# Performance work log

Hardware: AMD Instinct MI355X
Metric: run time of the kernel (lower is better)

## Reference

```python
import jax, jax.numpy as jnp
import numpy as np

N_NODES = 50000
N_EDGES = 800000
DIM_IN = 128
DIM_OUT = 64


def setup_inputs() -> dict:
    key = jax.random.key(0)
    k1, k2, k3, k4 = jax.random.split(key, 4)
    x = jax.random.normal(k1, (N_NODES, DIM_IN), dtype=jnp.float32)
    edge_index = jax.random.randint(k2, (2, N_EDGES), 0, N_NODES, dtype=jnp.int64)
    W = jax.random.normal(k3, (DIM_IN, DIM_OUT), dtype=jnp.float32) / np.sqrt(DIM_IN)
    b = jax.random.normal(k4, (DIM_OUT,), dtype=jnp.float32) * 0.01
    return {"x": x, "edge_index": edge_index, "W": W, "b": b}


def reference(x, edge_index, W, b):
    # Faithful PyG GCNConv: add self-loops, symmetric deg normalization,
    # linear transform then normalized scatter-add aggregation, then bias.
    N = x.shape[0]
    h = x @ W  # [N, dim_out] — transform before propagate (PyG order)

    loops = jnp.arange(N, dtype=edge_index.dtype)
    src = jnp.concatenate([edge_index[0], loops])  # [E+N]
    dst = jnp.concatenate([edge_index[1], loops])  # [E+N]

    ones = jnp.ones(src.shape[0], dtype=h.dtype)
    deg = jax.ops.segment_sum(ones, dst, num_segments=N)  # in-degree incl. self-loop
    dinv = jnp.where(deg > 0, jax.lax.rsqrt(deg), 0.0)
    norm = dinv[src] * dinv[dst]  # [E+N]

    msgs = h[src] * norm[:, None]  # gather + scale
    out = jax.ops.segment_sum(msgs, dst, num_segments=N) + b  # scatter-add
    return jax.nn.log_softmax(out, axis=1)
```

## Files before the change

### kernel.cpp

```cpp
#include <hip/hip_runtime.h>
#include <hip/hip_fp16.h>
#include <cstdint>
#include <cstddef>

#define N_NODES 50000
#define N_EDGES 800000
#define DIM_IN  128
#define DIM_OUT 64

#define BSHIFT  6
#define BNODES  64
#define NB      1024
#define NBK     ((N_NODES + BNODES - 1) / BNODES)
#define EB      4096
#define SORTB   ((N_EDGES + EB - 1) / EB)
#define NE4     (N_EDGES / 4)
#define CAPB    1280
#define GROWS   128

typedef _Float16 f16x8 __attribute__((ext_vector_type(8)));
typedef _Float16 f16x4 __attribute__((ext_vector_type(4)));
typedef float    f32x4 __attribute__((ext_vector_type(4)));

__global__ __launch_bounds__(256) void k_zero(int* __restrict__ gcnt) {
    const int i = blockIdx.x * 256 + threadIdx.x;
    if (i < NB) gcnt[i] = 0;
}

__global__ __launch_bounds__(256) void kF(const int* __restrict__ ei,
                                          int* __restrict__ gcnt,
                                          unsigned* __restrict__ pairs) {
    __shared__ int hcnt[NB];
    __shared__ int cur[NB];
    const int t = threadIdx.x, blk = blockIdx.x;
    for (int i = t; i < NB; i += 256) hcnt[i] = 0;
    __syncthreads();

    const int4* src4 = (const int4*)ei;
    const int4* dst4 = (const int4*)(ei + N_EDGES);
    const int g0 = blk * (EB / 4);

#pragma unroll
    for (int it = 0; it < EB / 1024; ++it) {
        const int g = g0 + it * 256 + t;
        if (g < NE4) {
            const int4 d = dst4[g];
            atomicAdd(&hcnt[d.x >> BSHIFT], 1);
            atomicAdd(&hcnt[d.y >> BSHIFT], 1);
            atomicAdd(&hcnt[d.z >> BSHIFT], 1);
            atomicAdd(&hcnt[d.w >> BSHIFT], 1);
        }
    }
    __syncthreads();

    for (int i = t; i < NB; i += 256) {
        const int c = hcnt[i];
        const int base = c ? atomicAdd(&gcnt[i], c) : 0;
        cur[i] = i * CAPB + base;
    }
    __syncthreads();

#pragma unroll
    for (int it = 0; it < EB / 1024; ++it) {
        const int g = g0 + it * 256 + t;
        if (g < NE4) {
            const int4 sv = src4[g];
            const int4 dv = dst4[g];
            int b, p;
            b = dv.x >> BSHIFT; p = atomicAdd(&cur[b], 1);
            if (p < b * CAPB + CAPB) pairs[p] = ((unsigned)sv.x << 16) | (unsigned)dv.x;
            b = dv.y >> BSHIFT; p = atomicAdd(&cur[b], 1);
            if (p < b * CAPB + CAPB) pairs[p] = ((unsigned)sv.y << 16) | (unsigned)dv.y;
            b = dv.z >> BSHIFT; p = atomicAdd(&cur[b], 1);
            if (p < b * CAPB + CAPB) pairs[p] = ((unsigned)sv.z << 16) | (unsigned)dv.z;
            b = dv.w >> BSHIFT; p = atomicAdd(&cur[b], 1);
            if (p < b * CAPB + CAPB) pairs[p] = ((unsigned)sv.w << 16) | (unsigned)dv.w;
        }
    }
}

__global__ __launch_bounds__(256) void kSort(const unsigned* __restrict__ pairs,
                                             const int* __restrict__ gcnt,
                                             unsigned short* __restrict__ csr,
                                             int2* __restrict__ nodeoff2,
                                             float* __restrict__ dinv) {
    __shared__ int cnt[BNODES];
    __shared__ int cur[BNODES];
    const int b = blockIdx.x, t = threadIdx.x;
    const int eb = b * CAPB;
    const int count = min(gcnt[b], CAPB);
    const int ee = eb + count;

    if (t < BNODES) cnt[t] = 0;
    __syncthreads();

    {
        int i = eb + t;
        for (; i + 768 < ee; i += 1024) {
            const unsigned p0 = pairs[i];
            const unsigned p1 = pairs[i + 256];
            const unsigned p2 = pairs[i + 512];
            const unsigned p3 = pairs[i + 768];
            atomicAdd(&cnt[p0 & (BNODES - 1)], 1);
            atomicAdd(&cnt[p1 & (BNODES - 1)], 1);
            atomicAdd(&cnt[p2 & (BNODES - 1)], 1);
            atomicAdd(&cnt[p3 & (BNODES - 1)], 1);
        }
        for (; i < ee; i += 256) atomicAdd(&cnt[pairs[i] & (BNODES - 1)], 1);
    }
    __syncthreads();

    if (t < 64) {
        const int lane = t;
        const int v = cnt[lane];
        int xs = v;
#pragma unroll
        for (int off = 1; off < 64; off <<= 1) {
            int y = __shfl_up(xs, off);
            if (lane >= off) xs += y;
        }
        const int excl = xs - v;
        cur[lane] = eb + excl;
        const int n = (b << BSHIFT) + lane;
        if (n < N_NODES) {
            nodeoff2[n] = make_int2(eb + excl, v);
            dinv[n] = rsqrtf((float)(v + 1));
        }
    }
    __syncthreads();

    {
        int i = eb + t;
        for (; i + 768 < ee; i += 1024) {
            const unsigned p0 = pairs[i];
            const unsigned p1 = pairs[i + 256];
            const unsigned p2 = pairs[i + 512];
            const unsigned p3 = pairs[i + 768];
            int q;
            q = atomicAdd(&cur[p0 & (BNODES - 1)], 1); csr[q] = (unsigned short)(p0 >> 16);
            q = atomicAdd(&cur[p1 & (BNODES - 1)], 1); csr[q] = (unsigned short)(p1 >> 16);
            q = atomicAdd(&cur[p2 & (BNODES - 1)], 1); csr[q] = (unsigned short)(p2 >> 16);
            q = atomicAdd(&cur[p3 & (BNODES - 1)], 1); csr[q] = (unsigned short)(p3 >> 16);
        }
        for (; i < ee; i += 256) {
            const unsigned p = pairs[i];
            const int q = atomicAdd(&cur[p & (BNODES - 1)], 1);
            csr[q] = (unsigned short)(p >> 16);
        }
    }
}

__global__ __launch_bounds__(256) void k_gemm(const float* __restrict__ x,
                                              const float* __restrict__ W,
                                              const float* __restrict__ dinv,
                                              __half* __restrict__ h) {
    const int t = threadIdx.x;
    const int w = t >> 6;
    const int l = t & 63;
    const int q = l >> 4;
    const int m16 = l & 15;

    f16x8 bf[4][4];
#pragma unroll
    for (int kc = 0; kc < 4; ++kc)
#pragma unroll
        for (int ct = 0; ct < 4; ++ct) {
            const float* wp = W + (size_t)(kc * 32 + q * 8) * DIM_OUT + ct * 16 + m16;
            f16x8 v;
#pragma unroll
            for (int j = 0; j < 8; ++j) v[j] = (_Float16)wp[(size_t)j * DIM_OUT];
            bf[kc][ct] = v;
        }

    const int base = blockIdx.x * GROWS + w * 32;
#pragma unroll
    for (int rt = 0; rt < 2; ++rt) {
        const int m0 = base + rt * 16;
        int mrow = m0 + m16;
        if (mrow >= N_NODES) mrow = N_NODES - 1;

        f16x8 af[4];
#pragma unroll
        for (int kc = 0; kc < 4; ++kc) {
            const float4* xp = (const float4*)(x + (size_t)mrow * DIM_IN + kc * 32 + q * 8);
            const float4 p0 = xp[0], p1 = xp[1];
            f16x8 a;
            a[0] = (_Float16)p0.x; a[1] = (_Float16)p0.y;
            a[2] = (_Float16)p0.z; a[3] = (_Float16)p0.w;
            a[4] = (_Float16)p1.x; a[5] = (_Float16)p1.y;
            a[6] = (_Float16)p1.z; a[7] = (_Float16)p1.w;
            af[kc] = a;
        }

        f32x4 acc[4];
#pragma unroll
        for (int ct = 0; ct < 4; ++ct) acc[ct] = (f32x4){0.f, 0.f, 0.f, 0.f};
#pragma unroll
        for (int kc = 0; kc < 4; ++kc)
#pragma unroll
            for (int ct = 0; ct < 4; ++ct)
                acc[ct] = __builtin_amdgcn_mfma_f32_16x16x32_f16(af[kc], bf[kc][ct], acc[ct], 0, 0, 0);

#pragma unroll
        for (int reg = 0; reg < 4; ++reg) {
            const int r = m0 + q * 4 + reg;
            if (r < N_NODES) {
                const float d = dinv[r];
#pragma unroll
                for (int ct = 0; ct < 4; ++ct)
                    h[(size_t)r * DIM_OUT + ct * 16 + m16] = __float2half(acc[ct][reg] * d);
            }
        }
    }
}

__global__ __launch_bounds__(256) void kE_agg(const int2* __restrict__ nodeoff2,
                                              const unsigned short* __restrict__ csr,
                                              const __half* __restrict__ h,
                                              const float* __restrict__ bvec,
                                              float* __restrict__ out) {
    const int t = threadIdx.x;
    const int qw = t >> 4, sl = t & 15;
    const int n = blockIdx.x * 16 + qw;
    const f16x4* __restrict__ h4 = (const f16x4*)h;

    const int2 off = nodeoff2[n];
    const int s0 = off.x, s1 = off.x + off.y;

    const f16x4 hv = h4[n * 16 + sl];
    float a0f = (float)hv[0], a1f = (float)hv[1], a2f = (float)hv[2], a3f = (float)hv[3];

    int i = s0;
    for (; i + 4 <= s1; i += 4) {
        const int c0 = csr[i + 0];
        const int c1 = csr[i + 1];
        const int c2 = csr[i + 2];
        const int c3 = csr[i + 3];
        const f16x4 v0 = h4[c0 * 16 + sl];
        const f16x4 v1 = h4[c1 * 16 + sl];
        const f16x4 v2 = h4[c2 * 16 + sl];
        const f16x4 v3 = h4[c3 * 16 + sl];
        a0f += (float)v0[0] + (float)v1[0] + (float)v2[0] + (float)v3[0];
        a1f += (float)v0[1] + (float)v1[1] + (float)v2[1] + (float)v3[1];
        a2f += (float)v0[2] + (float)v1[2] + (float)v2[2] + (float)v3[2];
        a3f += (float)v0[3] + (float)v1[3] + (float)v2[3] + (float)v3[3];
    }
    for (; i < s1; ++i) {
        const f16x4 v0 = h4[csr[i] * 16 + sl];
        a0f += (float)v0[0]; a1f += (float)v0[1]; a2f += (float)v0[2]; a3f += (float)v0[3];
    }

    const float4 bias = *(const float4*)&bvec[4 * sl];
    const float di = rsqrtf((float)(off.y + 1));
    float v0 = a0f * di + bias.x;
    float v1 = a1f * di + bias.y;
    float v2 = a2f * di + bias.z;
    float v3 = a3f * di + bias.w;

    float m = fmaxf(fmaxf(v0, v1), fmaxf(v2, v3));
#pragma unroll
    for (int off2 = 8; off2 > 0; off2 >>= 1) m = fmaxf(m, __shfl_xor(m, off2));
    float s = __expf(v0 - m) + __expf(v1 - m) + __expf(v2 - m) + __expf(v3 - m);
#pragma unroll
    for (int off2 = 8; off2 > 0; off2 >>= 1) s += __shfl_xor(s, off2);
    const float ls = __logf(s);

    float4 o;
    o.x = v0 - m - ls; o.y = v1 - m - ls; o.z = v2 - m - ls; o.w = v3 - m - ls;
    *(float4*)&out[(size_t)n * DIM_OUT + 4 * sl] = o;
}

extern "C" void kernel_launch(void* const* d_in, const int* in_sizes, int n_in,
                              void* d_out, int out_size, void* d_ws, size_t ws_size,
                              hipStream_t stream) {
    const float* x  = (const float*)d_in[0];
    const int*   ei = (const int*)d_in[1];
    const float* W  = (const float*)d_in[2];
    const float* b  = (const float*)d_in[3];
    float* out = (float*)d_out;

    char* ws = (char*)d_ws;
    __half*         h        = (__half*)ws;         ws += (size_t)N_NODES * DIM_OUT * sizeof(__half);
    float*          dinv     = (float*)ws;          ws += (size_t)N_NODES * sizeof(float);
    unsigned*       pairs    = (unsigned*)ws;       ws += (size_t)NB * CAPB * sizeof(unsigned);
    unsigned short* csr      = (unsigned short*)ws; ws += (size_t)NB * CAPB * sizeof(unsigned short);
    int2*           nodeoff2 = (int2*)ws;           ws += (size_t)N_NODES * sizeof(int2);
    int*            gcnt     = (int*)ws;            ws += (size_t)NB * sizeof(int);

    k_zero<<<(NB + 255) / 256, 256, 0, stream>>>(gcnt);
    kF    <<<SORTB, 256, 0, stream>>>(ei, gcnt, pairs);
    kSort <<<NBK, 256, 0, stream>>>(pairs, gcnt, csr, nodeoff2, dinv);
    k_gemm<<<(N_NODES + GROWS - 1) / GROWS, 256, 0, stream>>>(x, W, dinv, h);
    kE_agg<<<N_NODES / 16, 256, 0, stream>>>(nodeoff2, csr, h, b, out);
}
```

Measured before the change: 123.5 us.

## Fuse all GCN stages into one persistent cooperative kernel with grid syncs

Replaces the five separate launches (zero, bucket scatter, per-bucket sort, GEMM, aggregate) with one cooperative persistent kernel that loops over work units and uses grid.sync between phases. The bucket scatter and the GEMM now run in the same phase, and the dinv scaling of h moves into the sort phase as a read-modify-write pass. This removes launch gaps and lets the edge binning overlap the GEMM. In exchange it adds grid-wide barriers, an extra read and write of h, and a fixed grid of up to 3x256 blocks that may limit occupancy during the aggregation phase.

```diff
diff --git a/kernel.cpp b/kernel.cpp
--- a/kernel.cpp
+++ b/kernel.cpp
@@ -1,7 +1,10 @@
 #include <hip/hip_runtime.h>
 #include <hip/hip_fp16.h>
+#include <hip/hip_cooperative_groups.h>
 #include <cstdint>
 #include <cstddef>
+
+namespace cg = cooperative_groups;
 
 #define N_NODES 50000
 #define N_EDGES 800000
@@ -17,257 +20,278 @@
 #define NE4     (N_EDGES / 4)
 #define CAPB    1280
 #define GROWS   128
+#define GEMMB   ((N_NODES + GROWS - 1) / GROWS)
+#define P1UNITS (SORTB + GEMMB)
+#define NGROUP  (N_NODES / 16)
 
 typedef _Float16 f16x8 __attribute__((ext_vector_type(8)));
 typedef _Float16 f16x4 __attribute__((ext_vector_type(4)));
 typedef float    f32x4 __attribute__((ext_vector_type(4)));
 
-__global__ __launch_bounds__(256) void k_zero(int* __restrict__ gcnt) {
-    const int i = blockIdx.x * 256 + threadIdx.x;
-    if (i < NB) gcnt[i] = 0;
-}
-
-__global__ __launch_bounds__(256) void kF(const int* __restrict__ ei,
-                                          int* __restrict__ gcnt,
-                                          unsigned* __restrict__ pairs) {
-    __shared__ int hcnt[NB];
-    __shared__ int cur[NB];
-    const int t = threadIdx.x, blk = blockIdx.x;
-    for (int i = t; i < NB; i += 256) hcnt[i] = 0;
-    __syncthreads();
-
-    const int4* src4 = (const int4*)ei;
-    const int4* dst4 = (const int4*)(ei + N_EDGES);
-    const int g0 = blk * (EB / 4);
-
-#pragma unroll
-    for (int it = 0; it < EB / 1024; ++it) {
-        const int g = g0 + it * 256 + t;
-        if (g < NE4) {
-            const int4 d = dst4[g];
-            atomicAdd(&hcnt[d.x >> BSHIFT], 1);
-            atomicAdd(&hcnt[d.y >> BSHIFT], 1);
-            atomicAdd(&hcnt[d.z >> BSHIFT], 1);
-            atomicAdd(&hcnt[d.w >> BSHIFT], 1);
+__global__ __launch_bounds__(256, 3) void kFused(
+        const int* __restrict__ ei,
+        int* __restrict__ gcnt,
+        unsigned* __restrict__ pairs,
+        const float* __restrict__ x,
+        const float* __restrict__ W,
+        unsigned short* __restrict__ csr,
+        int2* __restrict__ nodeoff2,
+        __half* __restrict__ h,
+        const float* __restrict__ bvec,
+        float* __restrict__ out) {
+    cg::grid_group grid = cg::this_grid();
+    const int t = threadIdx.x;
+    const int blk = blockIdx.x;
+    const int gsz = (int)gridDim.x;
+
+    __shared__ int sA[NB];
+    __shared__ int sB[NB];
+
+    if (blk < 4) gcnt[blk * 256 + t] = 0;
+    grid.sync();
+
+    for (int u = blk; u < P1UNITS; u += gsz) {
+        if (u < SORTB) {
+            __syncthreads();
+            for (int i = t; i < NB; i += 256) sA[i] = 0;
+            __syncthreads();
+            const int4* src4 = (const int4*)ei;
+            const int4* dst4 = (const int4*)(ei + N_EDGES);
+            const int g0 = u * (EB / 4);
+#pragma unroll
+            for (int it = 0; it < EB / 1024; ++it) {
+                const int g = g0 + it * 256 + t;
+                if (g < NE4) {
+                    const int4 d = dst4[g];
+                    atomicAdd(&sA[d.x >> BSHIFT], 1);
+                    atomicAdd(&sA[d.y >> BSHIFT], 1);
+                    atomicAdd(&sA[d.z >> BSHIFT], 1);
+                    atomicAdd(&sA[d.w >> BSHIFT], 1);
+                }
+            }
+            __syncthreads();
+            for (int i = t; i < NB; i += 256) {
+                const int c = sA[i];
+                const int base = c ? atomicAdd(&gcnt[i], c) : 0;
+                sB[i] = i * CAPB + base;
+            }
+            __syncthreads();
+#pragma unroll
+            for (int it = 0; it < EB / 1024; ++it) {
+                const int g = g0 + it * 256 + t;
+                if (g < NE4) {
+                    const int4 sv = src4[g];
+                    const int4 dv = dst4[g];
+                    int b, p;
+                    b = dv.x >> BSHIFT; p = atomicAdd(&sB[b], 1);
+                    if (p < b * CAPB + CAPB) pairs[p] = ((unsigned)sv.x << 16) | (unsigned)dv.x;
+                    b = dv.y >> BSHIFT; p = atomicAdd(&sB[b], 1);
+                    if (p < b * CAPB + CAPB) pairs[p] = ((unsigned)sv.y << 16) | (unsigned)dv.y;
+                    b = dv.z >> BSHIFT; p = atomicAdd(&sB[b], 1);
+                    if (p < b * CAPB + CAPB) pairs[p] = ((unsigned)sv.z << 16) | (unsigned)dv.z;
+                    b = dv.w >> BSHIFT; p = atomicAdd(&sB[b], 1);
+                    if (p < b * CAPB + CAPB) pairs[p] = ((unsigned)sv.w << 16) | (unsigned)dv.w;
+                }
+            }
+            __syncthreads();
+        } else {
+            const int w = t >> 6;
+            const int l = t & 63;
+            const int q = l >> 4;
+            const int m16 = l & 15;
+
+            f16x8 bf[4][4];
+#pragma unroll
+            for (int kc = 0; kc < 4; ++kc)
+#pragma unroll
+                for (int ct = 0; ct < 4; ++ct) {
+                    const float* wp = W + (size_t)(kc * 32 + q * 8) * DIM_OUT + ct * 16 + m16;
+                    f16x8 v;
+#pragma unroll
+                    for (int j = 0; j < 8; ++j) v[j] = (_Float16)wp[(size_t)j * DIM_OUT];
+                    bf[kc][ct] = v;
+                }
+
+            const int base = (u - SORTB) * GROWS + w * 32;
+#pragma unroll
+            for (int rt = 0; rt < 2; ++rt) {
+                const int m0 = base + rt * 16;
+                int mrow = m0 + m16;
+                if (mrow >= N_NODES) mrow = N_NODES - 1;
+
+                f16x8 af[4];
+#pragma unroll
+                for (int kc = 0; kc < 4; ++kc) {
+                    const float4* xp = (const float4*)(x + (size_t)mrow * DIM_IN + kc * 32 + q * 8);
+                    const float4 p0 = xp[0], p1 = xp[1];
+                    f16x8 a;
+                    a[0] = (_Float16)p0.x; a[1] = (_Float16)p0.y;
+                    a[2] = (_Float16)p0.z; a[3] = (_Float16)p0.w;
+                    a[4] = (_Float16)p1.x; a[5] = (_Float16)p1.y;
+                    a[6] = (_Float16)p1.z; a[7] = (_Float16)p1.w;
+                    af[kc] = a;
+                }
+
+                f32x4 acc[4];
+#pragma unroll
+                for (int ct = 0; ct < 4; ++ct) acc[ct] = (f32x4){0.f, 0.f, 0.f, 0.f};
+#pragma unroll
+                for (int kc = 0; kc < 4; ++kc)
+#pragma unroll
+                    for (int ct = 0; ct < 4; ++ct)
+                        acc[ct] = __builtin_amdgcn_mfma_f32_16x16x32_f16(af[kc], bf[kc][ct], acc[ct], 0, 0, 0);
+
+#pragma unroll
+                for (int reg = 0; reg < 4; ++reg) {
+                    const int r = m0 + q * 4 + reg;
+                    if (r < N_NODES) {
+#pragma unroll
+                        for (int ct = 0; ct < 4; ++ct)
+                            h[(size_t)r * DIM_OUT + ct * 16 + m16] = __float2half(acc[ct][reg]);
+                    }
+                }
+            }
         }
     }
-    __syncthreads();
-
-    for (int i = t; i < NB; i += 256) {
-        const int c = hcnt[i];
-        const int base = c ? atomicAdd(&gcnt[i], c) : 0;
-        cur[i] = i * CAPB + base;
-    }
-    __syncthreads();
-
-#pragma unroll
-    for (int it = 0; it < EB / 1024; ++it) {
-        const int g = g0 + it * 256 + t;
-        if (g < NE4) {
-            const int4 sv = src4[g];
-            const int4 dv = dst4[g];
-            int b, p;
-            b = dv.x >> BSHIFT; p = atomicAdd(&cur[b], 1);
-            if (p < b * CAPB + CAPB) pairs[p] = ((unsigned)sv.x << 16) | (unsigned)dv.x;
-            b = dv.y >> BSHIFT; p = atomicAdd(&cur[b], 1);
-            if (p < b * CAPB + CAPB) pairs[p] = ((unsigned)sv.y << 16) | (unsigned)dv.y;
-            b = dv.z >> BSHIFT; p = atomicAdd(&cur[b], 1);
-            if (p < b * CAPB + CAPB) pairs[p] = ((unsigned)sv.z << 16) | (unsigned)dv.z;
-            b = dv.w >> BSHIFT; p = atomicAdd(&cur[b], 1);
-            if (p < b * CAPB + CAPB) pairs[p] = ((unsigned)sv.w << 16) | (unsigned)dv.w;
+    grid.sync();
+
+    {
+        int* cnt = sA;
+        int* cur = sA + BNODES;
+        float* sdinv = (float*)(sA + 2 * BNODES);
+        f16x4* h4w = (f16x4*)h;
+
+        for (int bb = blk; bb < NBK; bb += gsz) {
+            __syncthreads();
+            if (t < BNODES) cnt[t] = 0;
+            __syncthreads();
+
+            const int eb = bb * CAPB;
+            const int count = min(gcnt[bb], CAPB);
+            const int ee = eb + count;
+
+            {
+                int i = eb + t;
+                for (; i + 768 < ee; i += 1024) {
+                    const unsigned p0 = pairs[i];
+                    const unsigned p1 = pairs[i + 256];
+                    const unsigned p2 = pairs[i + 512];
+                    const unsigned p3 = pairs[i + 768];
+                    atomicAdd(&cnt[p0 & (BNODES - 1)], 1);
+                    atomicAdd(&cnt[p1 & (BNODES - 1)], 1);
+                    atomicAdd(&cnt[p2 & (BNODES - 1)], 1);
+                    atomicAdd(&cnt[p3 & (BNODES - 1)], 1);
+                }
+                for (; i < ee; i += 256) atomicAdd(&cnt[pairs[i] & (BNODES - 1)], 1);
+            }
+            __syncthreads();
+
+            if (t < 64) {
+                const int lane = t;
+                const int v = cnt[lane];
+                int xs = v;
+#pragma unroll
+                for (int off = 1; off < 64; off <<= 1) {
+                    int y = __shfl_up(xs, off);
+                    if (lane >= off) xs += y;
+                }
+                const int excl = xs - v;
+                cur[lane] = eb + excl;
+                sdinv[lane] = rsqrtf((float)(v + 1));
+                const int n = (bb << BSHIFT) + lane;
+                if (n < N_NODES) nodeoff2[n] = make_int2(eb + excl, v);
+            }
+            __syncthreads();
+
+            for (int idx = t; idx < BNODES * 16; idx += 256) {
+                const int r = idx >> 4;
+                const int n = (bb << BSHIFT) + r;
+                if (n < N_NODES) {
+                    const float d = sdinv[r];
+                    f16x4 v = h4w[n * 16 + (idx & 15)];
+                    v[0] = (_Float16)((float)v[0] * d);
+                    v[1] = (_Float16)((float)v[1] * d);
+                    v[2] = (_Float16)((float)v[2] * d);
+                    v[3] = (_Float16)((float)v[3] * d);
+                    h4w[n * 16 + (idx & 15)] = v;
+                }
+            }
+
+            {
+                int i = eb + t;
+                for (; i + 768 < ee; i += 1024) {
+                    const unsigned p0 = pairs[i];
+                    const unsigned p1 = pairs[i + 256];
+                    const unsigned p2 = pairs[i + 512];
+                    const unsigned p3 = pairs[i + 768];
+                    int q;
+                    q = atomicAdd(&cur[p0 & (BNODES - 1)], 1); csr[q] = (unsigned short)(p0 >> 16);
+                    q = atomicAdd(&cur[p1 & (BNODES - 1)], 1); csr[q] = (unsigned short)(p1 >> 16);
+                    q = atomicAdd(&cur[p2 & (BNODES - 1)], 1); csr[q] = (unsigned short)(p2 >> 16);
+                    q = atomicAdd(&cur[p3 & (BNODES - 1)], 1); csr[q] = (unsigned short)(p3 >> 16);
+                }
+                for (; i < ee; i += 256) {
+                    const unsigned p = pairs[i];
+                    const int q = atomicAdd(&cur[p & (BNODES - 1)], 1);
+                    csr[q] = (unsigned short)(p >> 16);
+                }
+            }
         }
     }
-}
-
-__global__ __launch_bounds__(256) void kSort(const unsigned* __restrict__ pairs,
-                                             const int* __restrict__ gcnt,
-                                             unsigned short* __restrict__ csr,
-                                             int2* __restrict__ nodeoff2,
-                                             float* __restrict__ dinv) {
-    __shared__ int cnt[BNODES];
-    __shared__ int cur[BNODES];
-    const int b = blockIdx.x, t = threadIdx.x;
-    const int eb = b * CAPB;
-    const int count = min(gcnt[b], CAPB);
-    const int ee = eb + count;
-
-    if (t < BNODES) cnt[t] = 0;
-    __syncthreads();
+    grid.sync();
 
     {
-        int i = eb + t;
-        for (; i + 768 < ee; i += 1024) {
-            const unsigned p0 = pairs[i];
-            const unsigned p1 = pairs[i + 256];
-            const unsigned p2 = pairs[i + 512];
-            const unsigned p3 = pairs[i + 768];
-            atomicAdd(&cnt[p0 & (BNODES - 1)], 1);
-            atomicAdd(&cnt[p1 & (BNODES - 1)], 1);
-            atomicAdd(&cnt[p2 & (BNODES - 1)], 1);
-            atomicAdd(&cnt[p3 & (BNODES - 1)], 1);
-        }
-        for (; i < ee; i += 256) atomicAdd(&cnt[pairs[i] & (BNODES - 1)], 1);
-    }
-    __syncthreads();
-
-    if (t < 64) {
-        const int lane = t;
-        const int v = cnt[lane];
-        int xs = v;
-#pragma unroll
-        for (int off = 1; off < 64; off <<= 1) {
-            int y = __shfl_up(xs, off);
-            if (lane >= off) xs += y;
-        }
-        const int excl = xs - v;
-        cur[lane] = eb + excl;
-        const int n = (b << BSHIFT) + lane;
-        if (n < N_NODES) {
-            nodeoff2[n] = make_int2(eb + excl, v);
-            dinv[n] = rsqrtf((float)(v + 1));
+        const int qw = t >> 4, sl = t & 15;
+        const f16x4* __restrict__ h4 = (const f16x4*)h;
+        const float4 bias = *(const float4*)&bvec[4 * sl];
+
+        for (int g = blk; g < NGROUP; g += gsz) {
+            const int n = g * 16 + qw;
+            const int2 off = nodeoff2[n];
+            const int s0 = off.x, s1 = off.x + off.y;
+
+            const f16x4 hv = h4[n * 16 + sl];
+            float a0f = (float)hv[0], a1f = (float)hv[1], a2f = (float)hv[2], a3f = (float)hv[3];
+
+            int i = s0;
+            for (; i + 4 <= s1; i += 4) {
+                const int c0 = csr[i + 0];
+                const int c1 = csr[i + 1];
+                const int c2 = csr[i + 2];
+                const int c3 = csr[i + 3];
+                const f16x4 v0 = h4[c0 * 16 + sl];
+                const f16x4 v1 = h4[c1 * 16 + sl];
+                const f16x4 v2 = h4[c2 * 16 + sl];
+                const f16x4 v3 = h4[c3 * 16 + sl];
+                a0f += (float)v0[0] + (float)v1[0] + (float)v2[0] + (float)v3[0];
+                a1f += (float)v0[1] + (float)v1[1] + (float)v2[1] + (float)v3[1];
+                a2f += (float)v0[2] + (float)v1[2] + (float)v2[2] + (float)v3[2];
+                a3f += (float)v0[3] + (float)v1[3] + (float)v2[3] + (float)v3[3];
+            }
+            for (; i < s1; ++i) {
+                const f16x4 v0 = h4[csr[i] * 16 + sl];
+                a0f += (float)v0[0]; a1f += (float)v0[1]; a2f += (float)v0[2]; a3f += (float)v0[3];
+            }
+
+            const float di = rsqrtf((float)(off.y + 1));
+            float v0 = a0f * di + bias.x;
+            float v1 = a1f * di + bias.y;
+            float v2 = a2f * di + bias.z;
+            float v3 = a3f * di + bias.w;
+
+            float m = fmaxf(fmaxf(v0, v1), fmaxf(v2, v3));
+#pragma unroll
+            for (int o = 8; o > 0; o >>= 1) m = fmaxf(m, __shfl_xor(m, o));
+            float s = __expf(v0 - m) + __expf(v1 - m) + __expf(v2 - m) + __expf(v3 - m);
+#pragma unroll
+            for (int o = 8; o > 0; o >>= 1) s += __shfl_xor(s, o);
+            const float ls = __logf(s);
+
+            float4 o4;
+            o4.x = v0 - m - ls; o4.y = v1 - m - ls; o4.z = v2 - m - ls; o4.w = v3 - m - ls;
+            *(float4*)&out[(size_t)n * DIM_OUT + 4 * sl] = o4;
         }
     }
-    __syncthreads();
-
-    {
-        int i = eb + t;
-        for (; i + 768 < ee; i += 1024) {
-            const unsigned p0 = pairs[i];
-            const unsigned p1 = pairs[i + 256];
-            const unsigned p2 = pairs[i + 512];
-            const unsigned p3 = pairs[i + 768];
-            int q;
-            q = atomicAdd(&cur[p0 & (BNODES - 1)], 1); csr[q] = (unsigned short)(p0 >> 16);
-            q = atomicAdd(&cur[p1 & (BNODES - 1)], 1); csr[q] = (unsigned short)(p1 >> 16);
-            q = atomicAdd(&cur[p2 & (BNODES - 1)], 1); csr[q] = (unsigned short)(p2 >> 16);
-            q = atomicAdd(&cur[p3 & (BNODES - 1)], 1); csr[q] = (unsigned short)(p3 >> 16);
-        }
-        for (; i < ee; i += 256) {
-            const unsigned p = pairs[i];
-            const int q = atomicAdd(&cur[p & (BNODES - 1)], 1);
-            csr[q] = (unsigned short)(p >> 16);
-        }
-    }
-}
-
-__global__ __launch_bounds__(256) void k_gemm(const float* __restrict__ x,
-                                              const float* __restrict__ W,
-                                              const float* __restrict__ dinv,
-                                              __half* __restrict__ h) {
-    const int t = threadIdx.x;
-    const int w = t >> 6;
-    const int l = t & 63;
-    const int q = l >> 4;
-    const int m16 = l & 15;
-
-    f16x8 bf[4][4];
-#pragma unroll
-    for (int kc = 0; kc < 4; ++kc)
-#pragma unroll
-        for (int ct = 0; ct < 4; ++ct) {
-            const float* wp = W + (size_t)(kc * 32 + q * 8) * DIM_OUT + ct * 16 + m16;
-            f16x8 v;
-#pragma unroll
-            for (int j = 0; j < 8; ++j) v[j] = (_Float16)wp[(size_t)j * DIM_OUT];
-            bf[kc][ct] = v;
-        }
-
-    const int base = blockIdx.x * GROWS + w * 32;
-#pragma unroll
-    for (int rt = 0; rt < 2; ++rt) {
-        const int m0 = base + rt * 16;
-        int mrow = m0 + m16;
-        if (mrow >= N_NODES) mrow = N_NODES - 1;
-
-        f16x8 af[4];
-#pragma unroll
-        for (int kc = 0; kc < 4; ++kc) {
-            const float4* xp = (const float4*)(x + (size_t)mrow * DIM_IN + kc * 32 + q * 8);
-            const float4 p0 = xp[0], p1 = xp[1];
-            f16x8 a;
-            a[0] = (_Float16)p0.x; a[1] = (_Float16)p0.y;
-            a[2] = (_Float16)p0.z; a[3] = (_Float16)p0.w;
-            a[4] = (_Float16)p1.x; a[5] = (_Float16)p1.y;
-            a[6] = (_Float16)p1.z; a[7] = (_Float16)p1.w;
-            af[kc] = a;
-        }
-
-        f32x4 acc[4];
-#pragma unroll
-        for (int ct = 0; ct < 4; ++ct) acc[ct] = (f32x4){0.f, 0.f, 0.f, 0.f};
-#pragma unroll
-        for (int kc = 0; kc < 4; ++kc)
-#pragma unroll
-            for (int ct = 0; ct < 4; ++ct)
-                acc[ct] = __builtin_amdgcn_mfma_f32_16x16x32_f16(af[kc], bf[kc][ct], acc[ct], 0, 0, 0);
-
-#pragma unroll
-        for (int reg = 0; reg < 4; ++reg) {
-            const int r = m0 + q * 4 + reg;
-            if (r < N_NODES) {
-                const float d = dinv[r];
-#pragma unroll
-                for (int ct = 0; ct < 4; ++ct)
-                    h[(size_t)r * DIM_OUT + ct * 16 + m16] = __float2half(acc[ct][reg] * d);
-            }
-        }
-    }
-}
-
-__global__ __launch_bounds__(256) void kE_agg(const int2* __restrict__ nodeoff2,
-                                              const unsigned short* __restrict__ csr,
-                                              const __half* __restrict__ h,
-                                              const float* __restrict__ bvec,
-                                              float* __restrict__ out) {
-    const int t = threadIdx.x;
-    const int qw = t >> 4, sl = t & 15;
-    const int n = blockIdx.x * 16 + qw;
-    const f16x4* __restrict__ h4 = (const f16x4*)h;
-
-    const int2 off = nodeoff2[n];
-    const int s0 = off.x, s1 = off.x + off.y;
-
-    const f16x4 hv = h4[n * 16 + sl];
-    float a0f = (float)hv[0], a1f = (float)hv[1], a2f = (float)hv[2], a3f = (float)hv[3];
-
-    int i = s0;
-    for (; i + 4 <= s1; i += 4) {
-        const int c0 = csr[i + 0];
-        const int c1 = csr[i + 1];
-        const int c2 = csr[i + 2];
-        const int c3 = csr[i + 3];
-        const f16x4 v0 = h4[c0 * 16 + sl];
-        const f16x4 v1 = h4[c1 * 16 + sl];
-        const f16x4 v2 = h4[c2 * 16 + sl];
-        const f16x4 v3 = h4[c3 * 16 + sl];
-        a0f += (float)v0[0] + (float)v1[0] + (float)v2[0] + (float)v3[0];
-        a1f += (float)v0[1] + (float)v1[1] + (float)v2[1] + (float)v3[1];
-        a2f += (float)v0[2] + (float)v1[2] + (float)v2[2] + (float)v3[2];
-        a3f += (float)v0[3] + (float)v1[3] + (float)v2[3] + (float)v3[3];
-    }
-    for (; i < s1; ++i) {
-        const f16x4 v0 = h4[csr[i] * 16 + sl];
-        a0f += (float)v0[0]; a1f += (float)v0[1]; a2f += (float)v0[2]; a3f += (float)v0[3];
-    }
-
-    const float4 bias = *(const float4*)&bvec[4 * sl];
-    const float di = rsqrtf((float)(off.y + 1));
-    float v0 = a0f * di + bias.x;
-    float v1 = a1f * di + bias.y;
-    float v2 = a2f * di + bias.z;
-    float v3 = a3f * di + bias.w;
-
-    float m = fmaxf(fmaxf(v0, v1), fmaxf(v2, v3));
-#pragma unroll
-    for (int off2 = 8; off2 > 0; off2 >>= 1) m = fmaxf(m, __shfl_xor(m, off2));
-    float s = __expf(v0 - m) + __expf(v1 - m) + __expf(v2 - m) + __expf(v3 - m);
-#pragma unroll
-    for (int off2 = 8; off2 > 0; off2 >>= 1) s += __shfl_xor(s, off2);
-    const float ls = __logf(s);
-
-    float4 o;
-    o.x = v0 - m - ls; o.y = v1 - m - ls; o.z = v2 - m - ls; o.w = v3 - m - ls;
-    *(float4*)&out[(size_t)n * DIM_OUT + 4 * sl] = o;
 }
 
 extern "C" void kernel_launch(void* const* d_in, const int* in_sizes, int n_in,
@@ -281,15 +305,19 @@
 
     char* ws = (char*)d_ws;
     __half*         h        = (__half*)ws;         ws += (size_t)N_NODES * DIM_OUT * sizeof(__half);
-    float*          dinv     = (float*)ws;          ws += (size_t)N_NODES * sizeof(float);
     unsigned*       pairs    = (unsigned*)ws;       ws += (size_t)NB * CAPB * sizeof(unsigned);
     unsigned short* csr      = (unsigned short*)ws; ws += (size_t)NB * CAPB * sizeof(unsigned short);
     int2*           nodeoff2 = (int2*)ws;           ws += (size_t)N_NODES * sizeof(int2);
     int*            gcnt     = (int*)ws;            ws += (size_t)NB * sizeof(int);
 
-    k_zero<<<(NB + 255) / 256, 256, 0, stream>>>(gcnt);
-    kF    <<<SORTB, 256, 0, stream>>>(ei, gcnt, pairs);
-    kSort <<<NBK, 256, 0, stream>>>(pairs, gcnt, csr, nodeoff2, dinv);
-    k_gemm<<<(N_NODES + GROWS - 1) / GROWS, 256, 0, stream>>>(x, W, dinv, h);
-    kE_agg<<<N_NODES / 16, 256, 0, stream>>>(nodeoff2, csr, h, b, out);
+    int maxb = 0;
+    (void)hipOccupancyMaxActiveBlocksPerMultiprocessor(&maxb, kFused, 256, 0);
+    if (maxb < 1) maxb = 1;
+    if (maxb > 3) maxb = 3;
+    const int grid = maxb * 256;
+
+    void* args[] = {(void*)&ei, (void*)&gcnt, (void*)&pairs, (void*)&x, (void*)&W,
+                    (void*)&csr, (void*)&nodeoff2, (void*)&h, (void*)&b, (void*)&out};
+    (void)hipLaunchCooperativeKernel((void*)kFused, dim3(grid), dim3(256),
+                                     args, 0, stream);
 }
```

Result: slower. 305.4 us (+147.2%).

## Fuse edge binning with GEMM and apply dinv scaling in sort kernel

Applied to the files above, without the earlier changes.

The edge-binning pass and the x@W GEMM now run as one launch, with block ranges split by blockIdx, so the independent GEMM can overlap the atomic-heavy binning. The GEMM no longer depends on dinv. The per-node dinv scaling of h moves into kSort, which computes degrees and rescales its 64 rows of h in place. The aggregation kernel now uses 8 lanes per node with f16x8 loads instead of 16 lanes with f16x4. This drops one launch and the dinv buffer, but adds a read-modify-write of h in kSort and a second fp16 rounding of h.

```diff
diff --git a/kernel.cpp b/kernel.cpp
--- a/kernel.cpp
+++ b/kernel.cpp
@@ -17,6 +17,8 @@
 #define NE4     (N_EDGES / 4)
 #define CAPB    1280
 #define GROWS   128
+#define GEMMB   ((N_NODES + GROWS - 1) / GROWS)
+#define NEGRP   ((N_NODES + 31) / 32)
 
 typedef _Float16 f16x8 __attribute__((ext_vector_type(8)));
 typedef _Float16 f16x4 __attribute__((ext_vector_type(4)));
@@ -27,54 +29,114 @@
     if (i < NB) gcnt[i] = 0;
 }
 
-__global__ __launch_bounds__(256) void kF(const int* __restrict__ ei,
-                                          int* __restrict__ gcnt,
-                                          unsigned* __restrict__ pairs) {
-    __shared__ int hcnt[NB];
-    __shared__ int cur[NB];
-    const int t = threadIdx.x, blk = blockIdx.x;
-    for (int i = t; i < NB; i += 256) hcnt[i] = 0;
-    __syncthreads();
-
-    const int4* src4 = (const int4*)ei;
-    const int4* dst4 = (const int4*)(ei + N_EDGES);
-    const int g0 = blk * (EB / 4);
-
-#pragma unroll
-    for (int it = 0; it < EB / 1024; ++it) {
-        const int g = g0 + it * 256 + t;
-        if (g < NE4) {
-            const int4 d = dst4[g];
-            atomicAdd(&hcnt[d.x >> BSHIFT], 1);
-            atomicAdd(&hcnt[d.y >> BSHIFT], 1);
-            atomicAdd(&hcnt[d.z >> BSHIFT], 1);
-            atomicAdd(&hcnt[d.w >> BSHIFT], 1);
-        }
-    }
-    __syncthreads();
-
-    for (int i = t; i < NB; i += 256) {
-        const int c = hcnt[i];
-        const int base = c ? atomicAdd(&gcnt[i], c) : 0;
-        cur[i] = i * CAPB + base;
-    }
-    __syncthreads();
-
-#pragma unroll
-    for (int it = 0; it < EB / 1024; ++it) {
-        const int g = g0 + it * 256 + t;
-        if (g < NE4) {
-            const int4 sv = src4[g];
-            const int4 dv = dst4[g];
-            int b, p;
-            b = dv.x >> BSHIFT; p = atomicAdd(&cur[b], 1);
-            if (p < b * CAPB + CAPB) pairs[p] = ((unsigned)sv.x << 16) | (unsigned)dv.x;
-            b = dv.y >> BSHIFT; p = atomicAdd(&cur[b], 1);
-            if (p < b * CAPB + CAPB) pairs[p] = ((unsigned)sv.y << 16) | (unsigned)dv.y;
-            b = dv.z >> BSHIFT; p = atomicAdd(&cur[b], 1);
-            if (p < b * CAPB + CAPB) pairs[p] = ((unsigned)sv.z << 16) | (unsigned)dv.z;
-            b = dv.w >> BSHIFT; p = atomicAdd(&cur[b], 1);
-            if (p < b * CAPB + CAPB) pairs[p] = ((unsigned)sv.w << 16) | (unsigned)dv.w;
+__global__ __launch_bounds__(256) void kFG(const int* __restrict__ ei,
+                                           int* __restrict__ gcnt,
+                                           unsigned* __restrict__ pairs,
+                                           const float* __restrict__ x,
+                                           const float* __restrict__ W,
+                                           __half* __restrict__ h) {
+    const int t = threadIdx.x;
+    if (blockIdx.x < SORTB) {
+        __shared__ int hcnt[NB];
+        __shared__ int cur[NB];
+        const int blk = blockIdx.x;
+        for (int i = t; i < NB; i += 256) hcnt[i] = 0;
+        __syncthreads();
+        const int4* src4 = (const int4*)ei;
+        const int4* dst4 = (const int4*)(ei + N_EDGES);
+        const int g0 = blk * (EB / 4);
+#pragma unroll
+        for (int it = 0; it < EB / 1024; ++it) {
+            const int g = g0 + it * 256 + t;
+            if (g < NE4) {
+                const int4 d = dst4[g];
+                atomicAdd(&hcnt[d.x >> BSHIFT], 1);
+                atomicAdd(&hcnt[d.y >> BSHIFT], 1);
+                atomicAdd(&hcnt[d.z >> BSHIFT], 1);
+                atomicAdd(&hcnt[d.w >> BSHIFT], 1);
+            }
+        }
+        __syncthreads();
+        for (int i = t; i < NB; i += 256) {
+            const int c = hcnt[i];
+            const int base = c ? atomicAdd(&gcnt[i], c) : 0;
+            cur[i] = i * CAPB + base;
+        }
+        __syncthreads();
+#pragma unroll
+        for (int it = 0; it < EB / 1024; ++it) {
+            const int g = g0 + it * 256 + t;
+            if (g < NE4) {
+                const int4 sv = src4[g];
+                const int4 dv = dst4[g];
+                int b, p;
+                b = dv.x >> BSHIFT; p = atomicAdd(&cur[b], 1);
+                if (p < b * CAPB + CAPB) pairs[p] = ((unsigned)sv.x << 16) | (unsigned)dv.x;
+                b = dv.y >> BSHIFT; p = atomicAdd(&cur[b], 1);
+                if (p < b * CAPB + CAPB) pairs[p] = ((unsigned)sv.y << 16) | (unsigned)dv.y;
+                b = dv.z >> BSHIFT; p = atomicAdd(&cur[b], 1);
+                if (p < b * CAPB + CAPB) pairs[p] = ((unsigned)sv.z << 16) | (unsigned)dv.z;
+                b = dv.w >> BSHIFT; p = atomicAdd(&cur[b], 1);
+                if (p < b * CAPB + CAPB) pairs[p] = ((unsigned)sv.w << 16) | (unsigned)dv.w;
+            }
+        }
+    } else {
+        const int u = blockIdx.x - SORTB;
+        const int w = t >> 6;
+        const int l = t & 63;
+        const int q = l >> 4;
+        const int m16 = l & 15;
+
+        f16x8 bf[4][4];
+#pragma unroll
+        for (int kc = 0; kc < 4; ++kc)
+#pragma unroll
+            for (int ct = 0; ct < 4; ++ct) {
+                const float* wp = W + (size_t)(kc * 32 + q * 8) * DIM_OUT + ct * 16 + m16;
+                f16x8 v;
+#pragma unroll
+                for (int j = 0; j < 8; ++j) v[j] = (_Float16)wp[(size_t)j * DIM_OUT];
+                bf[kc][ct] = v;
+            }
+
+        const int base = u * GROWS + w * 32;
+#pragma unroll
+        for (int rt = 0; rt < 2; ++rt) {
+            const int m0 = base + rt * 16;
+            int mrow = m0 + m16;
+            if (mrow >= N_NODES) mrow = N_NODES - 1;
+
+            f16x8 af[4];
+#pragma unroll
+            for (int kc = 0; kc < 4; ++kc) {
+                const float4* xp = (const float4*)(x + (size_t)mrow * DIM_IN + kc * 32 + q * 8);
+                const float4 p0 = xp[0], p1 = xp[1];
+                f16x8 a;
+                a[0] = (_Float16)p0.x; a[1] = (_Float16)p0.y;
+                a[2] = (_Float16)p0.z; a[3] = (_Float16)p0.w;
+                a[4] = (_Float16)p1.x; a[5] = (_Float16)p1.y;
+                a[6] = (_Float16)p1.z; a[7] = (_Float16)p1.w;
+                af[kc] = a;
+            }
+
+            f32x4 acc[4];
+#pragma unroll
+            for (int ct = 0; ct < 4; ++ct) acc[ct] = (f32x4){0.f, 0.f, 0.f, 0.f};
+#pragma unroll
+            for (int kc = 0; kc < 4; ++kc)
+#pragma unroll
+                for (int ct = 0; ct < 4; ++ct)
+                    acc[ct] = __builtin_amdgcn_mfma_f32_16x16x32_f16(af[kc], bf[kc][ct], acc[ct], 0, 0, 0);
+
+#pragma unroll
+            for (int reg = 0; reg < 4; ++reg) {
+                const int r = m0 + q * 4 + reg;
+                if (r < N_NODES) {
+#pragma unroll
+                    for (int ct = 0; ct < 4; ++ct)
+                        h[(size_t)r * DIM_OUT + ct * 16 + m16] = __float2half(acc[ct][reg]);
+                }
+            }
         }
     }
 }
@@ -83,9 +145,10 @@
                                              const int* __restrict__ gcnt,
                                              unsigned short* __restrict__ csr,
                                              int2* __restrict__ nodeoff2,
-                                             float* __restrict__ dinv) {
+                                             __half* __restrict__ h) {
     __shared__ int cnt[BNODES];
     __shared__ int cur[BNODES];
+    __shared__ float sdinv[BNODES];
     const int b = blockIdx.x, t = threadIdx.x;
     const int eb = b * CAPB;
     const int count = min(gcnt[b], CAPB);
@@ -121,13 +184,26 @@
         }
         const int excl = xs - v;
         cur[lane] = eb + excl;
+        sdinv[lane] = rsqrtf((float)(v + 1));
         const int n = (b << BSHIFT) + lane;
-        if (n < N_NODES) {
-            nodeoff2[n] = make_int2(eb + excl, v);
-            dinv[n] = rsqrtf((float)(v + 1));
-        }
+        if (n < N_NODES) nodeoff2[n] = make_int2(eb + excl, v);
     }
     __syncthreads();
+
+    {
+        f16x8* h8w = (f16x8*)h;
+        for (int idx = t; idx < BNODES * 8; idx += 256) {
+            const int r = idx >> 3;
+            const int n = (b << BSHIFT) + r;
+            if (n < N_NODES) {
+                const float d = sdinv[r];
+                f16x8 v = h8w[n * 8 + (idx & 7)];
+#pragma unroll
+                for (int j = 0; j < 8; ++j) v[j] = (_Float16)((float)v[j] * d);
+                h8w[n * 8 + (idx & 7)] = v;
+            }
+        }
+    }
 
     {
         int i = eb + t;
@@ -150,85 +226,24 @@
     }
 }
 
-__global__ __launch_bounds__(256) void k_gemm(const float* __restrict__ x,
-                                              const float* __restrict__ W,
-                                              const float* __restrict__ dinv,
-                                              __half* __restrict__ h) {
-    const int t = threadIdx.x;
-    const int w = t >> 6;
-    const int l = t & 63;
-    const int q = l >> 4;
-    const int m16 = l & 15;
-
-    f16x8 bf[4][4];
-#pragma unroll
-    for (int kc = 0; kc < 4; ++kc)
-#pragma unroll
-        for (int ct = 0; ct < 4; ++ct) {
-            const float* wp = W + (size_t)(kc * 32 + q * 8) * DIM_OUT + ct * 16 + m16;
-            f16x8 v;
-#pragma unroll
-            for (int j = 0; j < 8; ++j) v[j] = (_Float16)wp[(size_t)j * DIM_OUT];
-            bf[kc][ct] = v;
-        }
-
-    const int base = blockIdx.x * GROWS + w * 32;
-#pragma unroll
-    for (int rt = 0; rt < 2; ++rt) {
-        const int m0 = base + rt * 16;
-        int mrow = m0 + m16;
-        if (mrow >= N_NODES) mrow = N_NODES - 1;
-
-        f16x8 af[4];
-#pragma unroll
-        for (int kc = 0; kc < 4; ++kc) {
-            const float4* xp = (const float4*)(x + (size_t)mrow * DIM_IN + kc * 32 + q * 8);
-            const float4 p0 = xp[0], p1 = xp[1];
-            f16x8 a;
-            a[0] = (_Float16)p0.x; a[1] = (_Float16)p0.y;
-            a[2] = (_Float16)p0.z; a[3] = (_Float16)p0.w;
-            a[4] = (_Float16)p1.x; a[5] = (_Float16)p1.y;
-            a[6] = (_Float16)p1.z; a[7] = (_Float16)p1.w;
-            af[kc] = a;
-        }
-
-        f32x4 acc[4];
-#pragma unroll
-        for (int ct = 0; ct < 4; ++ct) acc[ct] = (f32x4){0.f, 0.f, 0.f, 0.f};
-#pragma unroll
-        for (int kc = 0; kc < 4; ++kc)
-#pragma unroll
-            for (int ct = 0; ct < 4; ++ct)
-                acc[ct] = __builtin_amdgcn_mfma_f32_16x16x32_f16(af[kc], bf[kc][ct], acc[ct], 0, 0, 0);
-
-#pragma unroll
-        for (int reg = 0; reg < 4; ++reg) {
-            const int r = m0 + q * 4 + reg;
-            if (r < N_NODES) {
-                const float d = dinv[r];
-#pragma unroll
-                for (int ct = 0; ct < 4; ++ct)
-                    h[(size_t)r * DIM_OUT + ct * 16 + m16] = __float2half(acc[ct][reg] * d);
-            }
-        }
-    }
-}
-
 __global__ __launch_bounds__(256) void kE_agg(const int2* __restrict__ nodeoff2,
                                               const unsigned short* __restrict__ csr,
                                               const __half* __restrict__ h,
                                               const float* __restrict__ bvec,
                                               float* __restrict__ out) {
     const int t = threadIdx.x;
-    const int qw = t >> 4, sl = t & 15;
-    const int n = blockIdx.x * 16 + qw;
-    const f16x4* __restrict__ h4 = (const f16x4*)h;
+    const int ew = t >> 3, sl = t & 7;
+    const int n = blockIdx.x * 32 + ew;
+    if (n >= N_NODES) return;
+    const f16x8* __restrict__ h8 = (const f16x8*)h;
 
     const int2 off = nodeoff2[n];
     const int s0 = off.x, s1 = off.x + off.y;
 
-    const f16x4 hv = h4[n * 16 + sl];
-    float a0f = (float)hv[0], a1f = (float)hv[1], a2f = (float)hv[2], a3f = (float)hv[3];
+    const f16x8 hv = h8[n * 8 + sl];
+    float a[8];
+#pragma unroll
+    for (int j = 0; j < 8; ++j) a[j] = (float)hv[j];
 
     int i = s0;
     for (; i + 4 <= s1; i += 4) {
@@ -236,38 +251,46 @@
         const int c1 = csr[i + 1];
         const int c2 = csr[i + 2];
         const int c3 = csr[i + 3];
-        const f16x4 v0 = h4[c0 * 16 + sl];
-        const f16x4 v1 = h4[c1 * 16 + sl];
-        const f16x4 v2 = h4[c2 * 16 + sl];
-        const f16x4 v3 = h4[c3 * 16 + sl];
-        a0f += (float)v0[0] + (float)v1[0] + (float)v2[0] + (float)v3[0];
-        a1f += (float)v0[1] + (float)v1[1] + (float)v2[1] + (float)v3[1];
-        a2f += (float)v0[2] + (float)v1[2] + (float)v2[2] + (float)v3[2];
-        a3f += (float)v0[3] + (float)v1[3] + (float)v2[3] + (float)v3[3];
+        const f16x8 v0 = h8[c0 * 8 + sl];
+        const f16x8 v1 = h8[c1 * 8 + sl];
+        const f16x8 v2 = h8[c2 * 8 + sl];
+        const f16x8 v3 = h8[c3 * 8 + sl];
+#pragma unroll
+        for (int j = 0; j < 8; ++j)
+            a[j] += (float)v0[j] + (float)v1[j] + (float)v2[j] + (float)v3[j];
     }
     for (; i < s1; ++i) {
-        const f16x4 v0 = h4[csr[i] * 16 + sl];
-        a0f += (float)v0[0]; a1f += (float)v0[1]; a2f += (float)v0[2]; a3f += (float)v0[3];
-    }
-
-    const float4 bias = *(const float4*)&bvec[4 * sl];
+        const f16x8 v0 = h8[csr[i] * 8 + sl];
+#pragma unroll
+        for (int j = 0; j < 8; ++j) a[j] += (float)v0[j];
+    }
+
+    const float4 b0 = *(const float4*)&bvec[8 * sl];
+    const float4 b1 = *(const float4*)&bvec[8 * sl + 4];
     const float di = rsqrtf((float)(off.y + 1));
-    float v0 = a0f * di + bias.x;
-    float v1 = a1f * di + bias.y;
-    float v2 = a2f * di + bias.z;
-    float v3 = a3f * di + bias.w;
-
-    float m = fmaxf(fmaxf(v0, v1), fmaxf(v2, v3));
-#pragma unroll
-    for (int off2 = 8; off2 > 0; off2 >>= 1) m = fmaxf(m, __shfl_xor(m, off2));
-    float s = __expf(v0 - m) + __expf(v1 - m) + __expf(v2 - m) + __expf(v3 - m);
-#pragma unroll
-    for (int off2 = 8; off2 > 0; off2 >>= 1) s += __shfl_xor(s, off2);
-    const float ls = __logf(s);
-
-    float4 o;
-    o.x = v0 - m - ls; o.y = v1 - m - ls; o.z = v2 - m - ls; o.w = v3 - m - ls;
-    *(float4*)&out[(size_t)n * DIM_OUT + 4 * sl] = o;
+    float v[8];
+    v[0] = a[0] * di + b0.x; v[1] = a[1] * di + b0.y;
+    v[2] = a[2] * di + b0.z; v[3] = a[3] * di + b0.w;
+    v[4] = a[4] * di + b1.x; v[5] = a[5] * di + b1.y;
+    v[6] = a[6] * di + b1.z; v[7] = a[7] * di + b1.w;
+
+    float m = v[0];
+#pragma unroll
+    for (int j = 1; j < 8; ++j) m = fmaxf(m, v[j]);
+#pragma unroll
+    for (int o = 4; o > 0; o >>= 1) m = fmaxf(m, __shfl_xor(m, o));
+    float s = 0.f;
+#pragma unroll
+    for (int j = 0; j < 8; ++j) s += __expf(v[j] - m);
+#pragma unroll
+    for (int o = 4; o > 0; o >>= 1) s += __shfl_xor(s, o);
+    const float ls = m + __logf(s);
+
+    float4 o0, o1;
+    o0.x = v[0] - ls; o0.y = v[1] - ls; o0.z = v[2] - ls; o0.w = v[3] - ls;
+    o1.x = v[4] - ls; o1.y = v[5] - ls; o1.z = v[6] - ls; o1.w = v[7] - ls;
+    *(float4*)&out[(size_t)n * DIM_OUT + 8 * sl]     = o0;
+    *(float4*)&out[(size_t)n * DIM_OUT + 8 * sl + 4] = o1;
 }
 
 extern "C" void kernel_launch(void* const* d_in, const int* in_sizes, int n_in,
@@ -281,15 +304,13 @@
 
     char* ws = (char*)d_ws;
     __half*         h        = (__half*)ws;         ws += (size_t)N_NODES * DIM_OUT * sizeof(__half);
-    float*          dinv     = (float*)ws;          ws += (size_t)N_NODES * sizeof(float);
     unsigned*       pairs    = (unsigned*)ws;       ws += (size_t)NB * CAPB * sizeof(unsigned);
     unsigned short* csr      = (unsigned short*)ws; ws += (size_t)NB * CAPB * sizeof(unsigned short);
     int2*           nodeoff2 = (int2*)ws;           ws += (size_t)N_NODES * sizeof(int2);
     int*            gcnt     = (int*)ws;            ws += (size_t)NB * sizeof(int);
 
     k_zero<<<(NB + 255) / 256, 256, 0, stream>>>(gcnt);
-    kF    <<<SORTB, 256, 0, stream>>>(ei, gcnt, pairs);
-    kSort <<<NBK, 256, 0, stream>>>(pairs, gcnt, csr, nodeoff2, dinv);
-    k_gemm<<<(N_NODES + GROWS - 1) / GROWS, 256, 0, stream>>>(x, W, dinv, h);
-    kE_agg<<<N_NODES / 16, 256, 0, stream>>>(nodeoff2, csr, h, b, out);
-}
+    kFG   <<<SORTB + GEMMB, 256, 0, stream>>>(ei, gcnt, pairs, x, W, h);
+    kSort <<<NBK, 256, 0, stream>>>(pairs, gcnt, csr, nodeoff2, h);
+    kE_agg<<<NEGRP, 256, 0, stream>>>(nodeoff2, csr, h, b, out);
+}
```

Measured after the change: 115.3 us. -6.7%, faster.
